# Kernel optimization log

Measured on AMD Instinct MI355X. Metric: run time of the kernel, lower is better.

The kernel has to match this reference:

```python
import jax, jax.numpy as jnp
import numpy as np
import math

IN_DIM = 768
FREQ = IN_DIM // 2 + 1          # 385
K = max(1, int(FREQ * 0.1))     # 38
MLP_IN = 2 * K                  # 76
HID = 256
LN_EPS = 1e-5


def _spectral_mask(task_id=0):
    # Faithful port of PiNoiseBiLoRA._get_spectral_mask
    avail = np.arange(1, FREQ)
    mt = 20
    idx = avail[task_id % mt::mt]
    if len(idx) >= K:
        idx = idx[:K]
    else:
        needed = K - len(idx)
        rf = math.ceil(needed / len(idx))
        idx = np.concatenate([idx, np.tile(idx, rf)[:needed]])
    return idx.astype(np.int32)


def setup_inputs() -> dict:
    key = jax.random.key(0)
    ks = jax.random.split(key, 6)
    B, S = 8, 4096
    x = jax.random.normal(ks[0], (B, S, IN_DIM), dtype=jnp.float32)
    eps = jax.random.normal(ks[1], (B, S, MLP_IN), dtype=jnp.float32)
    indices = jnp.asarray(_spectral_mask(0))
    w_scale = 0.05
    mu_w1 = jax.random.normal(ks[2], (HID, MLP_IN), dtype=jnp.float32) * w_scale
    mu_w2 = jax.random.normal(ks[3], (MLP_IN, HID), dtype=jnp.float32) * w_scale
    sg_w1 = jax.random.normal(ks[4], (HID, MLP_IN), dtype=jnp.float32) * w_scale
    sg_w2 = jax.random.normal(ks[5], (MLP_IN, HID), dtype=jnp.float32) * w_scale
    zeros_h = jnp.zeros((HID,), jnp.float32)
    zeros_o = jnp.zeros((MLP_IN,), jnp.float32)
    ones_h = jnp.ones((HID,), jnp.float32)
    return {
        'x': x, 'eps': eps, 'indices': indices,
        'mu_w1': mu_w1, 'mu_b1': zeros_h, 'mu_g': ones_h, 'mu_beta': zeros_h,
        'mu_w2': mu_w2, 'mu_b2': zeros_o,
        'sg_w1': sg_w1, 'sg_b1': zeros_h, 'sg_g': ones_h, 'sg_beta': zeros_h,
        'sg_w2': sg_w2, 'sg_b2': zeros_o,
    }


def _mlp(x, w1, b1, g, beta, w2, b2):
    # Linear -> LayerNorm -> GELU(exact) -> Linear
    h = x @ w1.T + b1
    mu = h.mean(axis=-1, keepdims=True)
    var = jnp.mean((h - mu) ** 2, axis=-1, keepdims=True)
    h = (h - mu) * jax.lax.rsqrt(var + LN_EPS) * g + beta
    h = jax.nn.gelu(h, approximate=False)
    return h @ w2.T + b2


def reference(x, eps, indices,
              mu_w1, mu_b1, mu_g, mu_beta, mu_w2, mu_b2,
              sg_w1, sg_b1, sg_g, sg_beta, sg_w2, sg_b2):
    # Training-mode forward of PiNoiseBiLoRA
    x_freq = jnp.fft.rfft(x, axis=-1)            # [B,S,FREQ] complex64
    x_sel = x_freq[..., indices]                 # gather k freq bins
    x_in = jnp.concatenate([x_sel.real, x_sel.imag], axis=-1)  # [B,S,2k]
    mu = _mlp(x_in, mu_w1, mu_b1, mu_g, mu_beta, mu_w2, mu_b2)
    sigma = _mlp(x_in, sg_w1, sg_b1, sg_g, sg_beta, sg_w2, sg_b2)
    z = mu + eps * sigma                         # reparameterization
    z_complex = jax.lax.complex(z[..., :K], z[..., K:]).astype(jnp.complex64)
    noise = jnp.zeros(x_freq.shape, jnp.complex64).at[..., indices].add(z_complex)
    return jnp.fft.irfft(noise, n=IN_DIM, axis=-1)
```

## Files before the change

kernel.cpp:

```cpp
#include <hip/hip_runtime.h>
#include <hip/hip_bf16.h>
#include <math.h>

#define INDIM 768
#define NROWS 32768
#define KSEL  38
#define NCOLS 76
#define HID   256
#define LN_EPS 1e-5f

typedef float  f32x4  __attribute__((ext_vector_type(4)));
typedef __bf16 bf16x8 __attribute__((ext_vector_type(8)));

#define MFMA16(a,b,c) __builtin_amdgcn_mfma_f32_16x16x32_bf16((a),(b),(c),0,0,0)

#define OFF_BFP 0
#define OFF_W1P 122880
#define OFF_W2P 221184
#define OFF_BSP 303104

__global__ void k_prep(const int* __restrict__ idxs,
                       const float* __restrict__ mu_w1, const float* __restrict__ sg_w1,
                       const float* __restrict__ mu_w2, const float* __restrict__ sg_w2,
                       __bf16* __restrict__ BfP, __bf16* __restrict__ W1P,
                       __bf16* __restrict__ W2P, __bf16* __restrict__ BsP)
{
    int tid = blockIdx.x * blockDim.x + threadIdx.x;
    int nth = gridDim.x * blockDim.x;
    const float TH = 6.28318530717958647692f / (float)INDIM;

    for (int e = tid; e < 120 * 512; e += nth) {
        int frag = e >> 9, lane = (e >> 3) & 63, j = e & 7;
        int kc = frag / 5, nt = frag % 5;
        int c = nt * 16 + (lane & 15);
        int k = kc * 32 + ((lane >> 4) << 3) + j;
        float v = 0.f;
        if (c < NCOLS) {
            int cc = (c < KSEL) ? c : c - KSEL;
            int f = idxs[cc];
            int m = (f * k) % INDIM;
            float s, co; sincosf(TH * (float)m, &s, &co);
            v = (c < KSEL) ? co : -s;
        }
        BfP[e] = (__bf16)v;
    }
    for (int e = tid; e < 96 * 512; e += nth) {
        int frag = e >> 9, lane = (e >> 3) & 63, j = e & 7;
        int mlp = frag / 48; int r = frag % 48;
        int nt = r / 3, ks = r % 3;
        int row = nt * 16 + (lane & 15);
        int k = ks * 32 + ((lane >> 4) << 3) + j;
        const float* W = mlp ? sg_w1 : mu_w1;
        W1P[e] = (__bf16)((k < NCOLS) ? W[row * NCOLS + k] : 0.f);
    }
    for (int e = tid; e < 80 * 512; e += nth) {
        int frag = e >> 9, lane = (e >> 3) & 63, j = e & 7;
        int mlp = frag / 40; int r = frag % 40;
        int nt = r / 8, ks = r % 8;
        int row = nt * 16 + (lane & 15);
        int k = ks * 32 + ((lane >> 4) << 3) + j;
        const float* W = mlp ? sg_w2 : mu_w2;
        W2P[e] = (__bf16)((row < NCOLS) ? W[row * HID + k] : 0.f);
    }
    for (int e = tid; e < 144 * 512; e += nth) {
        int frag = e >> 9, lane = (e >> 3) & 63, j = e & 7;
        int nt = frag / 3, ks = frag % 3;
        int n = nt * 16 + (lane & 15);
        int k = ks * 32 + ((lane >> 4) << 3) + j;
        float v = 0.f;
        if (k < NCOLS) {
            int cc = (k < KSEL) ? k : k - KSEL;
            int f = idxs[cc];
            int m = (f * n) % INDIM;
            float s, co; sincosf(TH * (float)m, &s, &co);
            v = ((k < KSEL) ? co : -s) * (2.0f / (float)INDIM);
        }
        BsP[e] = (__bf16)v;
    }
}

static __device__ inline float gelu_fast(float v) {
    float u = v * (0.79788456080286535588f + 0.03567740813636141f * v * v);
    return v / (1.f + __expf(-2.f * u));
}

static __device__ __forceinline__ void stage16(
    const __bf16* __restrict__ src, int nunits, char* dst, int w, int lane)
{
    typedef __attribute__((address_space(1))) const unsigned int g_u32;
    typedef __attribute__((address_space(3))) unsigned int l_u32;
    for (int u = w; u < nunits; u += 16)
        __builtin_amdgcn_global_load_lds((g_u32*)(src + (size_t)u * 512 + lane * 8),
                                         (l_u32*)(dst + u * 1024), 16, 0, 0);
}

__global__ __launch_bounds__(1024, 4) void k_fused(
    const float* __restrict__ x, const float* __restrict__ eps,
    const __bf16* __restrict__ Bf, const __bf16* __restrict__ W1f,
    const __bf16* __restrict__ W2f, const __bf16* __restrict__ Bs,
    const float* __restrict__ mu_b1, const float* __restrict__ mu_g,
    const float* __restrict__ mu_be, const float* __restrict__ mu_b2,
    const float* __restrict__ sg_b1, const float* __restrict__ sg_g,
    const float* __restrict__ sg_be, const float* __restrict__ sg_b2,
    float* __restrict__ out)
{
    __shared__ __align__(16) char   R[122880];
    __shared__ __align__(16) __bf16 tbuf[8][1664];
    float* PA = (float*)(R + 81920);

    int tid = threadIdx.x;
    int w = tid >> 6, lane = tid & 63, q = lane >> 4, l16 = lane & 15;
    int t = w >> 1, p = w & 1;
    int rbase = blockIdx.x * 128 + t * 16;

    f32x4 acc[5] = {};
    {
        const float* xrow = x + (size_t)(rbase + l16) * INDIM + p * 384 + q * 8;
        stage16(Bf, 120, R, w, lane);
        float4 f0 = ((const float4*)xrow)[0];
        float4 f1 = ((const float4*)xrow)[1];
        __syncthreads();
        #pragma unroll
        for (int kk = 0; kk < 12; ++kk) {
            float4 n0, n1;
            if (kk < 11) {
                n0 = ((const float4*)(xrow + (kk + 1) * 32))[0];
                n1 = ((const float4*)(xrow + (kk + 1) * 32))[1];
            }
            union { __bf16 h[8]; bf16x8 v; } a;
            a.h[0]=(__bf16)f0.x; a.h[1]=(__bf16)f0.y; a.h[2]=(__bf16)f0.z; a.h[3]=(__bf16)f0.w;
            a.h[4]=(__bf16)f1.x; a.h[5]=(__bf16)f1.y; a.h[6]=(__bf16)f1.z; a.h[7]=(__bf16)f1.w;
            const char* bb = R + (size_t)((p * 12 + kk) * 5) * 1024 + (size_t)lane * 16;
            #pragma unroll
            for (int nt = 0; nt < 5; ++nt) {
                bf16x8 b = *(const bf16x8*)(bb + nt * 1024);
                acc[nt] = MFMA16(a.v, b, acc[nt]);
            }
            if (kk < 11) { f0 = n0; f1 = n1; }
        }
    }
    __syncthreads();
    if (p == 1) {
        #pragma unroll
        for (int nt = 0; nt < 5; ++nt)
            #pragma unroll
            for (int r = 0; r < 4; ++r)
                PA[t * 1280 + (q * 4 + r) * 80 + nt * 16 + l16] = acc[nt][r];
    }
    __syncthreads();
    stage16(W1f, 80, R, w, lane);
    if (p == 0) {
        #pragma unroll
        for (int nt = 0; nt < 5; ++nt)
            #pragma unroll
            for (int r = 0; r < 4; ++r) {
                float v = acc[nt][r] + PA[t * 1280 + (q * 4 + r) * 80 + nt * 16 + l16];
                tbuf[t][(q * 4 + r) * 104 + nt * 16 + l16] = (__bf16)v;
            }
        #pragma unroll
        for (int r = 0; r < 4; ++r)
            tbuf[t][(q * 4 + r) * 104 + 80 + l16] = (__bf16)0.f;
    }
    __syncthreads();
    stage16(W1f + (size_t)80 * 512, 16, R + 81920, w, lane);
    bf16x8 a1[3];
    #pragma unroll
    for (int ks = 0; ks < 3; ++ks)
        a1[ks] = *(const bf16x8*)&tbuf[t][l16 * 104 + ks * 32 + q * 8];
    __syncthreads();

    const float* b1 = p ? sg_b1 : mu_b1;
    const float* g  = p ? sg_g  : mu_g;
    const float* be = p ? sg_be : mu_be;

    f32x4 h[16] = {};
    #pragma unroll
    for (int nt = 0; nt < 16; ++nt)
        #pragma unroll
        for (int ks = 0; ks < 3; ++ks) {
            bf16x8 b = *(const bf16x8*)(R + (size_t)((p * 48 + nt * 3 + ks) * 1024)
                                          + (size_t)lane * 16);
            h[nt] = MFMA16(a1[ks], b, h[nt]);
        }
    float s[4] = {}, ss[4] = {};
    #pragma unroll
    for (int nt = 0; nt < 16; ++nt) {
        float bb = b1[nt * 16 + l16];
        #pragma unroll
        for (int r = 0; r < 4; ++r) {
            float v = h[nt][r] + bb; h[nt][r] = v;
            s[r] += v; ss[r] += v * v;
        }
    }
    #pragma unroll
    for (int off = 1; off < 16; off <<= 1)
        #pragma unroll
        for (int r = 0; r < 4; ++r) {
            s[r] += __shfl_xor(s[r], off); ss[r] += __shfl_xor(ss[r], off);
        }
    float mean[4], rstd[4];
    #pragma unroll
    for (int r = 0; r < 4; ++r) {
        mean[r] = s[r] * (1.f / 256.f);
        rstd[r] = rsqrtf(ss[r] * (1.f / 256.f) - mean[r] * mean[r] + LN_EPS);
    }
    __syncthreads();
    stage16(W2f, 26, R + 71680, w, lane);
    stage16(W2f + (size_t)26 * 512, 24, R + 98304, w, lane);
    __bf16* gw = (__bf16*)R + w * 2176;
    bf16x8 a2[8];
    #pragma unroll
    for (int half = 0; half < 2; ++half) {
        #pragma unroll
        for (int ntl = 0; ntl < 8; ++ntl) {
            int nt = half * 8 + ntl;
            int i = nt * 16 + l16;
            float gv = g[i], bev = be[i];
            #pragma unroll
            for (int r = 0; r < 4; ++r)
                gw[(q * 4 + r) * 136 + ntl * 16 + l16] =
                    (__bf16)gelu_fast((h[nt][r] - mean[r]) * rstd[r] * gv + bev);
        }
        #pragma unroll
        for (int ks = 0; ks < 4; ++ks)
            a2[half * 4 + ks] = *(const bf16x8*)&gw[l16 * 136 + ks * 32 + q * 8];
    }
    __syncthreads();
    stage16(W2f + (size_t)50 * 512, 30, R, w, lane);
    __syncthreads();

    f32x4 o[5] = {};
    #pragma unroll
    for (int nt = 0; nt < 5; ++nt)
        #pragma unroll
        for (int ks = 0; ks < 8; ++ks) {
            int f = p * 40 + nt * 8 + ks;
            const char* base = (f < 26) ? (R + 71680 + f * 1024)
                             : (f < 50) ? (R + 98304 + (f - 26) * 1024)
                                        : (R + (f - 50) * 1024);
            bf16x8 b = *(const bf16x8*)(base + (size_t)lane * 16);
            o[nt] = MFMA16(a2[ks], b, o[nt]);
        }
    __syncthreads();

    stage16(Bs, 72, R, w, lane);
    float ev[5][4];
    if (p == 0) {
        #pragma unroll
        for (int nt = 0; nt < 5; ++nt)
            #pragma unroll
            for (int r = 0; r < 4; ++r)
                PA[t * 1280 + (q * 4 + r) * 80 + nt * 16 + l16] = o[nt][r];
    } else {
        #pragma unroll
        for (int nt = 0; nt < 5; ++nt) {
            int j = nt * 16 + l16;
            #pragma unroll
            for (int r = 0; r < 4; ++r)
                ev[nt][r] = (j < NCOLS)
                    ? eps[(size_t)(rbase + q * 4 + r) * NCOLS + j] : 0.f;
        }
    }
    __syncthreads();
    if (p == 1) {
        #pragma unroll
        for (int nt = 0; nt < 5; ++nt) {
            int j = nt * 16 + l16;
            float b2m = (j < NCOLS) ? mu_b2[j] : 0.f;
            float b2s = (j < NCOLS) ? sg_b2[j] : 0.f;
            #pragma unroll
            for (int r = 0; r < 4; ++r) {
                float z = 0.f;
                if (j < NCOLS) {
                    float omu = PA[t * 1280 + (q * 4 + r) * 80 + j];
                    z = (omu + b2m) + ev[nt][r] * (o[nt][r] + b2s);
                }
                tbuf[t][(q * 4 + r) * 104 + j] = (__bf16)z;
            }
        }
        #pragma unroll
        for (int r = 0; r < 4; ++r)
            tbuf[t][(q * 4 + r) * 104 + 80 + l16] = (__bf16)0.f;
    }
    __syncthreads();
    stage16(Bs + (size_t)72 * 512, 48, R + 73728, w, lane);
    bf16x8 az[3];
    #pragma unroll
    for (int ks = 0; ks < 3; ++ks)
        az[ks] = *(const bf16x8*)&tbuf[t][l16 * 104 + ks * 32 + q * 8];

    #pragma unroll
    for (int half = 0; half < 2; ++half) {
        if (half == 1) {
            __syncthreads();
            stage16(Bs + (size_t)120 * 512, 24, R, w, lane);
            __syncthreads();
        }
        #pragma unroll 4
        for (int c = 0; c < 12; ++c) {
            int ntl = p * 12 + c;
            int nt  = half * 24 + ntl;
            f32x4 oc = {};
            #pragma unroll
            for (int ks = 0; ks < 3; ++ks) {
                int idx = ntl * 3 + ks;
                const char* base;
                if (half == 0)       base = R + idx * 1024;
                else if (idx < 48)   base = R + 73728 + idx * 1024;
                else                 base = R + (idx - 48) * 1024;
                bf16x8 b = *(const bf16x8*)(base + (size_t)lane * 16);
                oc = MFMA16(az[ks], b, oc);
            }
            #pragma unroll
            for (int r = 0; r < 4; ++r)
                out[(size_t)(rbase + q * 4 + r) * INDIM + nt * 16 + l16] = oc[r];
        }
    }
}

extern "C" void kernel_launch(void* const* d_in, const int* in_sizes, int n_in,
                              void* d_out, int out_size, void* d_ws, size_t ws_size,
                              hipStream_t stream)
{
    const float* x     = (const float*)d_in[0];
    const float* eps   = (const float*)d_in[1];
    const int*   idxs  = (const int*)  d_in[2];
    const float* mu_w1 = (const float*)d_in[3];
    const float* mu_b1 = (const float*)d_in[4];
    const float* mu_g  = (const float*)d_in[5];
    const float* mu_be = (const float*)d_in[6];
    const float* mu_w2 = (const float*)d_in[7];
    const float* mu_b2 = (const float*)d_in[8];
    const float* sg_w1 = (const float*)d_in[9];
    const float* sg_b1 = (const float*)d_in[10];
    const float* sg_g  = (const float*)d_in[11];
    const float* sg_be = (const float*)d_in[12];
    const float* sg_w2 = (const float*)d_in[13];
    const float* sg_b2 = (const float*)d_in[14];
    float* out = (float*)d_out;

    char* ws = (char*)d_ws;
    __bf16* BfP = (__bf16*)(ws + OFF_BFP);
    __bf16* W1P = (__bf16*)(ws + OFF_W1P);
    __bf16* W2P = (__bf16*)(ws + OFF_W2P);
    __bf16* BsP = (__bf16*)(ws + OFF_BSP);

    hipLaunchKernelGGL(k_prep, dim3(1024), dim3(256), 0, stream,
                       idxs, mu_w1, sg_w1, mu_w2, sg_w2, BfP, W1P, W2P, BsP);
    hipLaunchKernelGGL(k_fused, dim3(NROWS / 128), dim3(1024), 0, stream,
                       x, eps, BfP, W1P, W2P, BsP,
                       mu_b1, mu_g, mu_be, mu_b2,
                       sg_b1, sg_g, sg_be, sg_b2, out);
}
```

Measured before the change: 238.0 us.

## Deduplicate repeated spectral bins to shrink DFT and first-layer GEMMs

The forward DFT basis now holds only the unique selected frequencies (24 instead of 38 per real/imag half), and the first MLP weight columns for duplicate bins are summed in the prep kernel. This cuts the DFT GEMM from 5 to 3 n-tiles and the first-layer K from 96 to 64. W2 staging is moved earlier and the second GEMM is split into two phases so a barrier and some staging latency overlap with compute. The unique-rank helpers run quadratic loops per element in the prep kernel, and the reduced padding assumes at most 24 unique bins, which holds for the default task id.

Measured after the change: 402.8 us. 69.2% more time.

```diff
diff --git a/kernel.cpp b/kernel.cpp
--- a/kernel.cpp
+++ b/kernel.cpp
@@ -15,9 +15,30 @@
 #define MFMA16(a,b,c) __builtin_amdgcn_mfma_f32_16x16x32_bf16((a),(b),(c),0,0,0)
 
 #define OFF_BFP 0
-#define OFF_W1P 122880
-#define OFF_W2P 221184
-#define OFF_BSP 303104
+#define OFF_W1P 73728
+#define OFF_W2P 139264
+#define OFF_BSP 221184
+
+static __device__ inline int rank_of(const int* idxs, int cc) {
+    int f = idxs[cc];
+    int p = 0; while (idxs[p] != f) ++p;
+    int rank = 0;
+    for (int a = 0; a < p; ++a) {
+        bool first = true;
+        for (int b = 0; b < a; ++b) if (idxs[b] == idxs[a]) { first = false; break; }
+        rank += first;
+    }
+    return rank;
+}
+static __device__ inline int freq_of_rank(const int* idxs, int tgt) {
+    int rank = 0;
+    for (int cc = 0; cc < KSEL; ++cc) {
+        bool first = true;
+        for (int b = 0; b < cc; ++b) if (idxs[b] == idxs[cc]) { first = false; break; }
+        if (first) { if (rank == tgt) return idxs[cc]; ++rank; }
+    }
+    return -1;
+}
 
 __global__ void k_prep(const int* __restrict__ idxs,
                        const float* __restrict__ mu_w1, const float* __restrict__ sg_w1,
@@ -29,29 +50,36 @@
     int nth = gridDim.x * blockDim.x;
     const float TH = 6.28318530717958647692f / (float)INDIM;
 
-    for (int e = tid; e < 120 * 512; e += nth) {
+    for (int e = tid; e < 72 * 512; e += nth) {
         int frag = e >> 9, lane = (e >> 3) & 63, j = e & 7;
-        int kc = frag / 5, nt = frag % 5;
-        int c = nt * 16 + (lane & 15);
+        int kc = frag / 3, nt = frag % 3;
+        int col = nt * 16 + (lane & 15);
         int k = kc * 32 + ((lane >> 4) << 3) + j;
+        int tgt = (col < 24) ? col : col - 24;
+        int f = freq_of_rank(idxs, tgt);
         float v = 0.f;
-        if (c < NCOLS) {
-            int cc = (c < KSEL) ? c : c - KSEL;
-            int f = idxs[cc];
+        if (f >= 0) {
             int m = (f * k) % INDIM;
             float s, co; sincosf(TH * (float)m, &s, &co);
-            v = (c < KSEL) ? co : -s;
+            v = (col < 24) ? co : -s;
         }
         BfP[e] = (__bf16)v;
     }
-    for (int e = tid; e < 96 * 512; e += nth) {
+    for (int e = tid; e < 64 * 512; e += nth) {
         int frag = e >> 9, lane = (e >> 3) & 63, j = e & 7;
-        int mlp = frag / 48; int r = frag % 48;
-        int nt = r / 3, ks = r % 3;
+        int mlp = frag / 32; int r = frag % 32;
+        int nt = r / 2, ks = r % 2;
         int row = nt * 16 + (lane & 15);
         int k = ks * 32 + ((lane >> 4) << 3) + j;
         const float* W = mlp ? sg_w1 : mu_w1;
-        W1P[e] = (__bf16)((k < NCOLS) ? W[row * NCOLS + k] : 0.f);
+        float v = 0.f;
+        if (k < 48) {
+            int tgt = (k < 24) ? k : k - 24;
+            int off = (k < 24) ? 0 : KSEL;
+            for (int cc = 0; cc < KSEL; ++cc)
+                if (rank_of(idxs, cc) == tgt) v += W[row * NCOLS + off + cc];
+        }
+        W1P[e] = (__bf16)v;
     }
     for (int e = tid; e < 80 * 512; e += nth) {
         int frag = e >> 9, lane = (e >> 3) & 63, j = e & 7;
@@ -106,17 +134,18 @@
 {
     __shared__ __align__(16) char   R[122880];
     __shared__ __align__(16) __bf16 tbuf[8][1664];
-    float* PA = (float*)(R + 81920);
+    float* PA1 = (float*)(R + 98304);
+    float* PA  = (float*)(R + 81920);
 
     int tid = threadIdx.x;
     int w = tid >> 6, lane = tid & 63, q = lane >> 4, l16 = lane & 15;
     int t = w >> 1, p = w & 1;
     int rbase = blockIdx.x * 128 + t * 16;
 
-    f32x4 acc[5] = {};
+    f32x4 acc[3] = {};
     {
         const float* xrow = x + (size_t)(rbase + l16) * INDIM + p * 384 + q * 8;
-        stage16(Bf, 120, R, w, lane);
+        stage16(Bf, 72, R, w, lane);
         float4 f0 = ((const float4*)xrow)[0];
         float4 f1 = ((const float4*)xrow)[1];
         __syncthreads();
@@ -130,44 +159,43 @@
             union { __bf16 h[8]; bf16x8 v; } a;
             a.h[0]=(__bf16)f0.x; a.h[1]=(__bf16)f0.y; a.h[2]=(__bf16)f0.z; a.h[3]=(__bf16)f0.w;
             a.h[4]=(__bf16)f1.x; a.h[5]=(__bf16)f1.y; a.h[6]=(__bf16)f1.z; a.h[7]=(__bf16)f1.w;
-            const char* bb = R + (size_t)((p * 12 + kk) * 5) * 1024 + (size_t)lane * 16;
-            #pragma unroll
-            for (int nt = 0; nt < 5; ++nt) {
+            const char* bb = R + (size_t)((p * 12 + kk) * 3) * 1024 + (size_t)lane * 16;
+            #pragma unroll
+            for (int nt = 0; nt < 3; ++nt) {
                 bf16x8 b = *(const bf16x8*)(bb + nt * 1024);
                 acc[nt] = MFMA16(a.v, b, acc[nt]);
             }
             if (kk < 11) { f0 = n0; f1 = n1; }
         }
     }
-    __syncthreads();
     if (p == 1) {
         #pragma unroll
-        for (int nt = 0; nt < 5; ++nt)
-            #pragma unroll
-            for (int r = 0; r < 4; ++r)
-                PA[t * 1280 + (q * 4 + r) * 80 + nt * 16 + l16] = acc[nt][r];
-    }
-    __syncthreads();
-    stage16(W1f, 80, R, w, lane);
+        for (int nt = 0; nt < 3; ++nt)
+            #pragma unroll
+            for (int r = 0; r < 4; ++r)
+                PA1[t * 768 + (q * 4 + r) * 48 + nt * 16 + l16] = acc[nt][r];
+    }
+    __syncthreads();
+    stage16(W1f, 64, R, w, lane);
     if (p == 0) {
         #pragma unroll
-        for (int nt = 0; nt < 5; ++nt)
+        for (int nt = 0; nt < 3; ++nt)
             #pragma unroll
             for (int r = 0; r < 4; ++r) {
-                float v = acc[nt][r] + PA[t * 1280 + (q * 4 + r) * 80 + nt * 16 + l16];
+                float v = acc[nt][r] + PA1[t * 768 + (q * 4 + r) * 48 + nt * 16 + l16];
                 tbuf[t][(q * 4 + r) * 104 + nt * 16 + l16] = (__bf16)v;
             }
         #pragma unroll
         for (int r = 0; r < 4; ++r)
-            tbuf[t][(q * 4 + r) * 104 + 80 + l16] = (__bf16)0.f;
-    }
-    __syncthreads();
-    stage16(W1f + (size_t)80 * 512, 16, R + 81920, w, lane);
-    bf16x8 a1[3];
-    #pragma unroll
-    for (int ks = 0; ks < 3; ++ks)
+            tbuf[t][(q * 4 + r) * 104 + 48 + l16] = (__bf16)0.f;
+    }
+    __syncthreads();
+    bf16x8 a1[2];
+    #pragma unroll
+    for (int ks = 0; ks < 2; ++ks)
         a1[ks] = *(const bf16x8*)&tbuf[t][l16 * 104 + ks * 32 + q * 8];
-    __syncthreads();
+    stage16(W2f, 26, R + 71680, w, lane);
+    stage16(W2f + (size_t)26 * 512, 24, R + 98304, w, lane);
 
     const float* b1 = p ? sg_b1 : mu_b1;
     const float* g  = p ? sg_g  : mu_g;
@@ -177,8 +205,8 @@
     #pragma unroll
     for (int nt = 0; nt < 16; ++nt)
         #pragma unroll
-        for (int ks = 0; ks < 3; ++ks) {
-            bf16x8 b = *(const bf16x8*)(R + (size_t)((p * 48 + nt * 3 + ks) * 1024)
+        for (int ks = 0; ks < 2; ++ks) {
+            bf16x8 b = *(const bf16x8*)(R + (size_t)((p * 32 + nt * 2 + ks) * 1024)
                                           + (size_t)lane * 16);
             h[nt] = MFMA16(a1[ks], b, h[nt]);
         }
@@ -205,8 +233,6 @@
         rstd[r] = rsqrtf(ss[r] * (1.f / 256.f) - mean[r] * mean[r] + LN_EPS);
     }
     __syncthreads();
-    stage16(W2f, 26, R + 71680, w, lane);
-    stage16(W2f + (size_t)26 * 512, 24, R + 98304, w, lane);
     __bf16* gw = (__bf16*)R + w * 2176;
     bf16x8 a2[8];
     #pragma unroll
@@ -227,7 +253,6 @@
     }
     __syncthreads();
     stage16(W2f + (size_t)50 * 512, 30, R, w, lane);
-    __syncthreads();
 
     f32x4 o[5] = {};
     #pragma unroll
@@ -235,11 +260,23 @@
         #pragma unroll
         for (int ks = 0; ks < 8; ++ks) {
             int f = p * 40 + nt * 8 + ks;
-            const char* base = (f < 26) ? (R + 71680 + f * 1024)
-                             : (f < 50) ? (R + 98304 + (f - 26) * 1024)
-                                        : (R + (f - 50) * 1024);
-            bf16x8 b = *(const bf16x8*)(base + (size_t)lane * 16);
-            o[nt] = MFMA16(a2[ks], b, o[nt]);
+            if (f < 50) {
+                const char* base = (f < 26) ? (R + 71680 + f * 1024)
+                                            : (R + 98304 + (f - 26) * 1024);
+                bf16x8 b = *(const bf16x8*)(base + (size_t)lane * 16);
+                o[nt] = MFMA16(a2[ks], b, o[nt]);
+            }
+        }
+    __syncthreads();
+    #pragma unroll
+    for (int nt = 0; nt < 5; ++nt)
+        #pragma unroll
+        for (int ks = 0; ks < 8; ++ks) {
+            int f = p * 40 + nt * 8 + ks;
+            if (f >= 50) {
+                bf16x8 b = *(const bf16x8*)(R + (f - 50) * 1024 + (size_t)lane * 16);
+                o[nt] = MFMA16(a2[ks], b, o[nt]);
+            }
         }
     __syncthreads();
 
```
